# Performance work log

Measured on AMD Instinct MI355X. Metric: run time of the kernel, lower is better.

## Reference

```python
import jax, jax.numpy as jnp
import numpy as np

N = 8192
F_X = 48       # raw node feature dim
F_RW = 16      # random-walk feature dim
IN_DIM = F_X + F_RW   # 64
H1 = 128
H2 = 64
N_BRANCH = 4   # hop0 (identity) + hop1..hop3


def setup_inputs() -> dict:
    key = jax.random.key(0)
    ks = jax.random.split(key, 9)
    x = jax.random.normal(ks[0], (N, F_X), dtype=jnp.float32)
    walk_feats = jax.random.normal(ks[1], (N, F_RW), dtype=jnp.float32)
    hop1 = jax.random.uniform(ks[2], (N, N), dtype=jnp.float32)
    hop2 = jax.random.uniform(ks[3], (N, N), dtype=jnp.float32)
    hop3 = jax.random.uniform(ks[4], (N, N), dtype=jnp.float32)
    # Stacked params for the 4 parallel 2-layer MLPs (layer0..layer3)
    s1 = 1.0 / np.sqrt(IN_DIM)
    s2 = 1.0 / np.sqrt(H1)
    W1 = jax.random.uniform(ks[5], (N_BRANCH, IN_DIM, H1), dtype=jnp.float32, minval=-s1, maxval=s1)
    b1 = jax.random.uniform(ks[6], (N_BRANCH, H1), dtype=jnp.float32, minval=-s1, maxval=s1)
    W2 = jax.random.uniform(ks[7], (N_BRANCH, H1, H2), dtype=jnp.float32, minval=-s2, maxval=s2)
    b2 = jax.random.uniform(ks[8], (N_BRANCH, H2), dtype=jnp.float32, minval=-s2, maxval=s2)
    return {"x": x, "walk_feats": walk_feats, "hop1": hop1, "hop2": hop2,
            "hop3": hop3, "W1": W1, "b1": b1, "W2": W2, "b2": b2}


def reference(x, walk_feats, hop1, hop2, hop3, W1, b1, W2, b2):
    # X = cat(x, walk_feats) along feature dim (use_rw=True)
    X = jnp.concatenate([x, walk_feats], axis=1)          # [N, IN_DIM]
    # Branch inputs: hop0 uses X directly; hops 1-3 aggregate via adjacency matmul
    hops = jnp.stack([X, hop1 @ X, hop2 @ X, hop3 @ X])   # [4, N, IN_DIM]
    # Parallel 2-layer MLPs: Linear -> ReLU -> Linear, per branch k
    h = jax.nn.relu(jnp.einsum('knf,kfh->knh', hops, W1) + b1[:, None, :])  # [4, N, H1]
    out = jnp.einsum('knh,kho->kno', h, W2) + b2[:, None, :]                 # [4, N, H2]
    return out.sum(axis=0)                                                   # [N, H2]
```

## Files before the change

kernel.cpp:

```cpp
#include <hip/hip_runtime.h>
#include <stdint.h>


#define N_NODES 8192
#define NDIM 64

typedef __attribute__((ext_vector_type(8))) short short8;
typedef __attribute__((ext_vector_type(4))) float f32x4;

__device__ __forceinline__ unsigned int f2bf(float f) {
  unsigned int u = __builtin_bit_cast(unsigned int, f);
  u += 0x7fffu + ((u >> 16) & 1u);
  return u >> 16;
}

__global__ void prep_kernel(const float* __restrict__ x,
                            const float* __restrict__ wf,
                            unsigned short* __restrict__ Bp) {
  int s = blockIdx.x * 256 + threadIdx.x;
  int khi = s >> 9;
  int rem = s & 511;
  int n   = rem >> 3;
  int klo = rem & 7;
  int k   = (khi << 3) | klo;
  float v = (n < 48) ? x[k * 48 + n] : wf[k * 16 + (n - 48)];
  Bp[s] = (unsigned short)f2bf(v);
}

__global__ void hop_gemm(const float* __restrict__ hop1,
                         const float* __restrict__ hop2,
                         const float* __restrict__ hop3,
                         const unsigned short* __restrict__ Bp,
                         float* __restrict__ Y) {
  int bid  = blockIdx.x;
  int h    = bid % 3;
  int mblk = bid / 3;
  const float* A = (h == 0) ? hop1 : (h == 1) ? hop2 : hop3;

  int tid  = threadIdx.x;
  int wave = tid >> 6;
  int lane = tid & 63;
  int n0   = lane & 15;
  int q    = lane >> 4;

  int rowA = mblk * 32 + wave * 16 + n0;
  const float* Arow = A + (size_t)rowA * N_NODES + q * 8;
  const short8* Bp8 = (const short8*)Bp;

  f32x4 acc0 = {0.f, 0.f, 0.f, 0.f};
  f32x4 acc1 = {0.f, 0.f, 0.f, 0.f};
  f32x4 acc2 = {0.f, 0.f, 0.f, 0.f};
  f32x4 acc3 = {0.f, 0.f, 0.f, 0.f};

#pragma unroll 4
  for (int k0 = 0; k0 < N_NODES; k0 += 32) {
    float4 a0 = *(const float4*)(Arow + k0);
    float4 a1 = *(const float4*)(Arow + k0 + 4);
    union { short8 s; unsigned int u[4]; } af;
    af.u[0] = (f2bf(a0.y) << 16) | f2bf(a0.x);
    af.u[1] = (f2bf(a0.w) << 16) | f2bf(a0.z);
    af.u[2] = (f2bf(a1.y) << 16) | f2bf(a1.x);
    af.u[3] = (f2bf(a1.w) << 16) | f2bf(a1.z);

    int bc = ((k0 >> 3) + q) * 64 + n0;
    short8 b0 = Bp8[bc];
    short8 b1 = Bp8[bc + 16];
    short8 b2 = Bp8[bc + 32];
    short8 b3 = Bp8[bc + 48];

    acc0 = __builtin_amdgcn_mfma_f32_16x16x32_bf16(af.s, b0, acc0, 0, 0, 0);
    acc1 = __builtin_amdgcn_mfma_f32_16x16x32_bf16(af.s, b1, acc1, 0, 0, 0);
    acc2 = __builtin_amdgcn_mfma_f32_16x16x32_bf16(af.s, b2, acc2, 0, 0, 0);
    acc3 = __builtin_amdgcn_mfma_f32_16x16x32_bf16(af.s, b3, acc3, 0, 0, 0);
  }

  float* Yo = Y + (size_t)h * (N_NODES * NDIM);
  int rowT = mblk * 32 + wave * 16 + 4 * q;
#pragma unroll
  for (int r = 0; r < 4; ++r) {
    float* yr = Yo + (size_t)(rowT + r) * NDIM + n0;
    yr[0]  = acc0[r];
    yr[16] = acc1[r];
    yr[32] = acc2[r];
    yr[48] = acc3[r];
  }
}

__global__ __launch_bounds__(256) void mlp_kernel(
    const float* __restrict__ x, const float* __restrict__ wf,
    const float* __restrict__ Y,
    const float* __restrict__ W1, const float* __restrict__ b1,
    const float* __restrict__ W2, const float* __restrict__ b2,
    float* __restrict__ out) {
  __shared__ __attribute__((aligned(16))) float Ys[32 * 64];
  __shared__ __attribute__((aligned(16))) float Ws[128 * 64];
  __shared__ __attribute__((aligned(16))) float Hs[32 * 128];
  __shared__ __attribute__((aligned(16))) float b1s[128];
  __shared__ __attribute__((aligned(16))) float b2s[64];

  int t = threadIdx.x;
  int rowBase = blockIdx.x * 32;

  int rg = t >> 5;
  int fg = t & 31;
  int rg2 = t >> 4;
  int cg  = t & 15;

  float oacc[2][4];
#pragma unroll
  for (int i = 0; i < 2; ++i)
#pragma unroll
    for (int j = 0; j < 4; ++j) oacc[i][j] = 0.f;

  for (int k = 0; k < 4; ++k) {
    for (int i = t; i < 32 * 64; i += 256) {
      float v;
      if (k == 0) {
        int row = rowBase + (i >> 6);
        int n = i & 63;
        v = (n < 48) ? x[row * 48 + n] : wf[row * 16 + (n - 48)];
      } else {
        v = Y[(size_t)(k - 1) * (N_NODES * 64) + (size_t)rowBase * 64 + i];
      }
      Ys[i] = v;
    }
    for (int i = t; i < 8192; i += 256) Ws[i] = W1[k * 8192 + i];
    if (t < 128) b1s[t] = b1[k * 128 + t];
    if (t >= 128 && t < 192) b2s[t - 128] = b2[k * 64 + (t - 128)];
    __syncthreads();

    float4 hacc[4];
#pragma unroll
    for (int i = 0; i < 4; ++i) hacc[i] = make_float4(0.f, 0.f, 0.f, 0.f);
    for (int kk = 0; kk < 64; ++kk) {
      float4 wv = *(const float4*)&Ws[kk * 128 + fg * 4];
#pragma unroll
      for (int i = 0; i < 4; ++i) {
        float yv = Ys[(rg * 4 + i) * 64 + kk];
        hacc[i].x = fmaf(yv, wv.x, hacc[i].x);
        hacc[i].y = fmaf(yv, wv.y, hacc[i].y);
        hacc[i].z = fmaf(yv, wv.z, hacc[i].z);
        hacc[i].w = fmaf(yv, wv.w, hacc[i].w);
      }
    }
    float4 bv = *(const float4*)&b1s[fg * 4];
#pragma unroll
    for (int i = 0; i < 4; ++i) {
      float4 hv;
      hv.x = fmaxf(hacc[i].x + bv.x, 0.f);
      hv.y = fmaxf(hacc[i].y + bv.y, 0.f);
      hv.z = fmaxf(hacc[i].z + bv.z, 0.f);
      hv.w = fmaxf(hacc[i].w + bv.w, 0.f);
      *(float4*)&Hs[(rg * 4 + i) * 128 + fg * 4] = hv;
    }
    __syncthreads();

    for (int i = t; i < 8192; i += 256) Ws[i] = W2[k * 8192 + i];
    __syncthreads();

    float o[2][4];
#pragma unroll
    for (int i = 0; i < 2; ++i) {
      float4 b2v = *(const float4*)&b2s[cg * 4];
      o[i][0] = b2v.x; o[i][1] = b2v.y; o[i][2] = b2v.z; o[i][3] = b2v.w;
    }
    for (int kk = 0; kk < 128; ++kk) {
      float4 wv = *(const float4*)&Ws[kk * 64 + cg * 4];
#pragma unroll
      for (int i = 0; i < 2; ++i) {
        float hv = Hs[(rg2 * 2 + i) * 128 + kk];
        o[i][0] = fmaf(hv, wv.x, o[i][0]);
        o[i][1] = fmaf(hv, wv.y, o[i][1]);
        o[i][2] = fmaf(hv, wv.z, o[i][2]);
        o[i][3] = fmaf(hv, wv.w, o[i][3]);
      }
    }
#pragma unroll
    for (int i = 0; i < 2; ++i)
#pragma unroll
      for (int j = 0; j < 4; ++j) oacc[i][j] += o[i][j];
    __syncthreads();
  }

#pragma unroll
  for (int i = 0; i < 2; ++i) {
    float4 v;
    v.x = oacc[i][0]; v.y = oacc[i][1]; v.z = oacc[i][2]; v.w = oacc[i][3];
    *(float4*)&out[(size_t)(rowBase + rg2 * 2 + i) * 64 + cg * 4] = v;
  }
}

extern "C" void kernel_launch(void* const* d_in, const int* in_sizes, int n_in,
                              void* d_out, int out_size, void* d_ws, size_t ws_size,
                              hipStream_t stream) {
  const float* x    = (const float*)d_in[0];
  const float* wf   = (const float*)d_in[1];
  const float* hop1 = (const float*)d_in[2];
  const float* hop2 = (const float*)d_in[3];
  const float* hop3 = (const float*)d_in[4];
  const float* W1   = (const float*)d_in[5];
  const float* b1   = (const float*)d_in[6];
  const float* W2   = (const float*)d_in[7];
  const float* b2   = (const float*)d_in[8];
  float* out = (float*)d_out;

  unsigned short* Bp = (unsigned short*)d_ws;
  float* Y = (float*)((char*)d_ws + (1 << 20));

  prep_kernel<<<dim3(524288 / 256), dim3(256), 0, stream>>>(x, wf, Bp);
  hop_gemm<<<dim3(768), dim3(128), 0, stream>>>(hop1, hop2, hop3, Bp, Y);
  mlp_kernel<<<dim3(256), dim3(256), 0, stream>>>(x, wf, Y, W1, b1, W2, b2, out);
}
```

Measured before the change: 883.3 us.

## Split hop GEMM K across waves with LDS reduction and double-buffered loads

```diff
diff --git a/kernel.cpp b/kernel.cpp
--- a/kernel.cpp
+++ b/kernel.cpp
@@ -27,167 +27,195 @@
   Bp[s] = (unsigned short)f2bf(v);
 }
 
-__global__ void hop_gemm(const float* __restrict__ hop1,
-                         const float* __restrict__ hop2,
-                         const float* __restrict__ hop3,
-                         const unsigned short* __restrict__ Bp,
-                         float* __restrict__ Y) {
+__global__ __launch_bounds__(256, 6) void hop_gemm(
+    const float* __restrict__ hop1,
+    const float* __restrict__ hop2,
+    const float* __restrict__ hop3,
+    const unsigned short* __restrict__ Bp,
+    float* __restrict__ Y) {
+  __shared__ __attribute__((aligned(16))) float red[4 * 1024];
+
   int bid  = blockIdx.x;
   int h    = bid % 3;
   int mblk = bid / 3;
   const float* A = (h == 0) ? hop1 : (h == 1) ? hop2 : hop3;
 
   int tid  = threadIdx.x;
-  int wave = tid >> 6;
+  int w    = tid >> 6;
   int lane = tid & 63;
   int n0   = lane & 15;
   int q    = lane >> 4;
 
-  int rowA = mblk * 32 + wave * 16 + n0;
-  const float* Arow = A + (size_t)rowA * N_NODES + q * 8;
-  const short8* Bp8 = (const short8*)Bp;
+  int rowA = mblk * 16 + n0;
+  const float* Arow = A + (size_t)rowA * N_NODES + w * 2048 + q * 8;
+  const short8* Bw  = (const short8*)Bp + ((size_t)(w * 256 + q)) * 64 + n0;
 
   f32x4 acc0 = {0.f, 0.f, 0.f, 0.f};
   f32x4 acc1 = {0.f, 0.f, 0.f, 0.f};
   f32x4 acc2 = {0.f, 0.f, 0.f, 0.f};
   f32x4 acc3 = {0.f, 0.f, 0.f, 0.f};
 
-#pragma unroll 4
-  for (int k0 = 0; k0 < N_NODES; k0 += 32) {
-    float4 a0 = *(const float4*)(Arow + k0);
-    float4 a1 = *(const float4*)(Arow + k0 + 4);
-    union { short8 s; unsigned int u[4]; } af;
-    af.u[0] = (f2bf(a0.y) << 16) | f2bf(a0.x);
-    af.u[1] = (f2bf(a0.w) << 16) | f2bf(a0.z);
-    af.u[2] = (f2bf(a1.y) << 16) | f2bf(a1.x);
-    af.u[3] = (f2bf(a1.w) << 16) | f2bf(a1.z);
-
-    int bc = ((k0 >> 3) + q) * 64 + n0;
-    short8 b0 = Bp8[bc];
-    short8 b1 = Bp8[bc + 16];
-    short8 b2 = Bp8[bc + 32];
-    short8 b3 = Bp8[bc + 48];
-
-    acc0 = __builtin_amdgcn_mfma_f32_16x16x32_bf16(af.s, b0, acc0, 0, 0, 0);
-    acc1 = __builtin_amdgcn_mfma_f32_16x16x32_bf16(af.s, b1, acc1, 0, 0, 0);
-    acc2 = __builtin_amdgcn_mfma_f32_16x16x32_bf16(af.s, b2, acc2, 0, 0, 0);
-    acc3 = __builtin_amdgcn_mfma_f32_16x16x32_bf16(af.s, b3, acc3, 0, 0, 0);
-  }
-
-  float* Yo = Y + (size_t)h * (N_NODES * NDIM);
-  int rowT = mblk * 32 + wave * 16 + 4 * q;
-#pragma unroll
-  for (int r = 0; r < 4; ++r) {
-    float* yr = Yo + (size_t)(rowT + r) * NDIM + n0;
-    yr[0]  = acc0[r];
-    yr[16] = acc1[r];
-    yr[32] = acc2[r];
-    yr[48] = acc3[r];
-  }
-}
-
+  float4 xa0, xa1, ya0, ya1;
+  short8 xb0, xb1, xb2, xb3;
+  short8 yb0, yb1, yb2, yb3;
+
+#define LOAD_A(s, A0, A1)                                \
+  do {                                                   \
+    const float* _p = Arow + 32 * (s);                   \
+    A0 = *(const float4*)_p;                             \
+    A1 = *(const float4*)(_p + 4);                       \
+  } while (0)
+
+#define LOAD_B(s, B0, B1, B2, B3)                        \
+  do {                                                   \
+    const short8* _p = Bw + 256 * (s);                   \
+    B0 = _p[0]; B1 = _p[16]; B2 = _p[32]; B3 = _p[48];   \
+  } while (0)
+
+#define PROC(A0, A1, B0, B1, B2, B3)                                        \
+  do {                                                                      \
+    union { short8 s; unsigned int u[4]; } af;                              \
+    af.u[0] = (f2bf((A0).y) << 16) | f2bf((A0).x);                          \
+    af.u[1] = (f2bf((A0).w) << 16) | f2bf((A0).z);                          \
+    af.u[2] = (f2bf((A1).y) << 16) | f2bf((A1).x);                          \
+    af.u[3] = (f2bf((A1).w) << 16) | f2bf((A1).z);                          \
+    acc0 = __builtin_amdgcn_mfma_f32_16x16x32_bf16(af.s, B0, acc0, 0, 0, 0);\
+    acc1 = __builtin_amdgcn_mfma_f32_16x16x32_bf16(af.s, B1, acc1, 0, 0, 0);\
+    acc2 = __builtin_amdgcn_mfma_f32_16x16x32_bf16(af.s, B2, acc2, 0, 0, 0);\
+    acc3 = __builtin_amdgcn_mfma_f32_16x16x32_bf16(af.s, B3, acc3, 0, 0, 0);\
+  } while (0)
+
+  LOAD_A(0, xa0, xa1);
+  LOAD_B(0, xb0, xb1, xb2, xb3);
+#pragma unroll 1
+  for (int s = 0; s < 62; s += 2) {
+    LOAD_A(s + 1, ya0, ya1);
+    LOAD_B(s + 1, yb0, yb1, yb2, yb3);
+    PROC(xa0, xa1, xb0, xb1, xb2, xb3);
+    LOAD_A(s + 2, xa0, xa1);
+    LOAD_B(s + 2, xb0, xb1, xb2, xb3);
+    PROC(ya0, ya1, yb0, yb1, yb2, yb3);
+  }
+  LOAD_A(63, ya0, ya1);
+  LOAD_B(63, yb0, yb1, yb2, yb3);
+  PROC(xa0, xa1, xb0, xb1, xb2, xb3);
+  PROC(ya0, ya1, yb0, yb1, yb2, yb3);
+
+#undef LOAD_A
+#undef LOAD_B
+#undef PROC
+
+  {
+    float* rw = &red[w * 1024 + lane * 4];
+    *(f32x4*)(rw)       = acc0;
+    *(f32x4*)(rw + 256) = acc1;
+    *(f32x4*)(rw + 512) = acc2;
+    *(f32x4*)(rw + 768) = acc3;
+  }
+  __syncthreads();
+
+  {
+    int t = tid;
+    f32x4 v = *(const f32x4*)&red[t * 4];
+    v += *(const f32x4*)&red[1024 + t * 4];
+    v += *(const f32x4*)&red[2048 + t * 4];
+    v += *(const f32x4*)&red[3072 + t * 4];
+
+    int nt    = t >> 6;
+    int lane2 = t & 63;
+    int q2    = lane2 >> 4;
+    int n02   = lane2 & 15;
+    int col   = nt * 16 + n02;
+    float* Yo = Y + (size_t)h * (N_NODES * NDIM)
+                  + (size_t)(mblk * 16 + q2 * 4) * NDIM + col;
+    Yo[0 * NDIM] = v.x;
+    Yo[1 * NDIM] = v.y;
+    Yo[2 * NDIM] = v.z;
+    Yo[3 * NDIM] = v.w;
+  }
+}
+
+#define YS_LD 68
+#define HS_LD 132
 __global__ __launch_bounds__(256) void mlp_kernel(
     const float* __restrict__ x, const float* __restrict__ wf,
     const float* __restrict__ Y,
     const float* __restrict__ W1, const float* __restrict__ b1,
     const float* __restrict__ W2, const float* __restrict__ b2,
     float* __restrict__ out) {
-  __shared__ __attribute__((aligned(16))) float Ys[32 * 64];
-  __shared__ __attribute__((aligned(16))) float Ws[128 * 64];
-  __shared__ __attribute__((aligned(16))) float Hs[32 * 128];
-  __shared__ __attribute__((aligned(16))) float b1s[128];
-  __shared__ __attribute__((aligned(16))) float b2s[64];
+  __shared__ __attribute__((aligned(16))) float Ys[16 * YS_LD];
+  __shared__ __attribute__((aligned(16))) float Hs[16 * HS_LD];
+  __shared__ float b1s[128];
+  __shared__ float b2s[64];
 
   int t = threadIdx.x;
-  int rowBase = blockIdx.x * 32;
-
-  int rg = t >> 5;
-  int fg = t & 31;
-  int rg2 = t >> 4;
-  int cg  = t & 15;
-
-  float oacc[2][4];
-#pragma unroll
-  for (int i = 0; i < 2; ++i)
-#pragma unroll
-    for (int j = 0; j < 4; ++j) oacc[i][j] = 0.f;
+  int rowBase = blockIdx.x * 16;
+
+  int r  = t >> 4;
+  int c8 = (t & 15) * 8;
+  int c4 = (t & 15) * 4;
+
+  float oacc[4] = {0.f, 0.f, 0.f, 0.f};
 
   for (int k = 0; k < 4; ++k) {
-    for (int i = t; i < 32 * 64; i += 256) {
+    for (int i = t; i < 16 * 64; i += 256) {
+      int row = i >> 6;
+      int n   = i & 63;
       float v;
       if (k == 0) {
-        int row = rowBase + (i >> 6);
-        int n = i & 63;
-        v = (n < 48) ? x[row * 48 + n] : wf[row * 16 + (n - 48)];
+        int grow = rowBase + row;
+        v = (n < 48) ? x[grow * 48 + n] : wf[grow * 16 + (n - 48)];
       } else {
-        v = Y[(size_t)(k - 1) * (N_NODES * 64) + (size_t)rowBase * 64 + i];
+        v = Y[(size_t)(k - 1) * (N_NODES * 64) + (size_t)(rowBase + row) * 64 + n];
       }
-      Ys[i] = v;
-    }
-    for (int i = t; i < 8192; i += 256) Ws[i] = W1[k * 8192 + i];
+      Ys[row * YS_LD + n] = v;
+    }
     if (t < 128) b1s[t] = b1[k * 128 + t];
-    if (t >= 128 && t < 192) b2s[t - 128] = b2[k * 64 + (t - 128)];
+    else if (t < 192) b2s[t - 128] = b2[k * 64 + (t - 128)];
     __syncthreads();
 
-    float4 hacc[4];
-#pragma unroll
-    for (int i = 0; i < 4; ++i) hacc[i] = make_float4(0.f, 0.f, 0.f, 0.f);
+    const float* W1k = W1 + k * 8192;
+    float f0 = 0.f, f1 = 0.f, f2 = 0.f, f3 = 0.f;
+    float f4 = 0.f, f5 = 0.f, f6 = 0.f, f7 = 0.f;
+#pragma unroll 4
     for (int kk = 0; kk < 64; ++kk) {
-      float4 wv = *(const float4*)&Ws[kk * 128 + fg * 4];
-#pragma unroll
-      for (int i = 0; i < 4; ++i) {
-        float yv = Ys[(rg * 4 + i) * 64 + kk];
-        hacc[i].x = fmaf(yv, wv.x, hacc[i].x);
-        hacc[i].y = fmaf(yv, wv.y, hacc[i].y);
-        hacc[i].z = fmaf(yv, wv.z, hacc[i].z);
-        hacc[i].w = fmaf(yv, wv.w, hacc[i].w);
-      }
-    }
-    float4 bv = *(const float4*)&b1s[fg * 4];
-#pragma unroll
-    for (int i = 0; i < 4; ++i) {
-      float4 hv;
-      hv.x = fmaxf(hacc[i].x + bv.x, 0.f);
-      hv.y = fmaxf(hacc[i].y + bv.y, 0.f);
-      hv.z = fmaxf(hacc[i].z + bv.z, 0.f);
-      hv.w = fmaxf(hacc[i].w + bv.w, 0.f);
-      *(float4*)&Hs[(rg * 4 + i) * 128 + fg * 4] = hv;
+      float yv = Ys[r * YS_LD + kk];
+      float4 w0 = *(const float4*)&W1k[kk * 128 + c8];
+      float4 w1 = *(const float4*)&W1k[kk * 128 + c8 + 4];
+      f0 = fmaf(yv, w0.x, f0); f1 = fmaf(yv, w0.y, f1);
+      f2 = fmaf(yv, w0.z, f2); f3 = fmaf(yv, w0.w, f3);
+      f4 = fmaf(yv, w1.x, f4); f5 = fmaf(yv, w1.y, f5);
+      f6 = fmaf(yv, w1.z, f6); f7 = fmaf(yv, w1.w, f7);
+    }
+    {
+      float4 ba = *(const float4*)&b1s[c8];
+      float4 bb = *(const float4*)&b1s[c8 + 4];
+      float4 h0, h1;
+      h0.x = fmaxf(f0 + ba.x, 0.f); h0.y = fmaxf(f1 + ba.y, 0.f);
+      h0.z = fmaxf(f2 + ba.z, 0.f); h0.w = fmaxf(f3 + ba.w, 0.f);
+      h1.x = fmaxf(f4 + bb.x, 0.f); h1.y = fmaxf(f5 + bb.y, 0.f);
+      h1.z = fmaxf(f6 + bb.z, 0.f); h1.w = fmaxf(f7 + bb.w, 0.f);
+      *(float4*)&Hs[r * HS_LD + c8]     = h0;
+      *(float4*)&Hs[r * HS_LD + c8 + 4] = h1;
     }
     __syncthreads();
 
-    for (int i = t; i < 8192; i += 256) Ws[i] = W2[k * 8192 + i];
+    const float* W2k = W2 + k * 8192;
+    float o0 = b2s[c4], o1 = b2s[c4 + 1], o2 = b2s[c4 + 2], o3 = b2s[c4 + 3];
+#pragma unroll 4
+    for (int kk = 0; kk < 128; ++kk) {
+      float hv = Hs[r * HS_LD + kk];
+      float4 wv = *(const float4*)&W2k[kk * 64 + c4];
+      o0 = fmaf(hv, wv.x, o0); o1 = fmaf(hv, wv.y, o1);
+      o2 = fmaf(hv, wv.z, o2); o3 = fmaf(hv, wv.w, o3);
+    }
+    oacc[0] += o0; oacc[1] += o1; oacc[2] += o2; oacc[3] += o3;
     __syncthreads();
-
-    float o[2][4];
-#pragma unroll
-    for (int i = 0; i < 2; ++i) {
-      float4 b2v = *(const float4*)&b2s[cg * 4];
-      o[i][0] = b2v.x; o[i][1] = b2v.y; o[i][2] = b2v.z; o[i][3] = b2v.w;
-    }
-    for (int kk = 0; kk < 128; ++kk) {
-      float4 wv = *(const float4*)&Ws[kk * 64 + cg * 4];
-#pragma unroll
-      for (int i = 0; i < 2; ++i) {
-        float hv = Hs[(rg2 * 2 + i) * 128 + kk];
-        o[i][0] = fmaf(hv, wv.x, o[i][0]);
-        o[i][1] = fmaf(hv, wv.y, o[i][1]);
-        o[i][2] = fmaf(hv, wv.z, o[i][2]);
-        o[i][3] = fmaf(hv, wv.w, o[i][3]);
-      }
-    }
-#pragma unroll
-    for (int i = 0; i < 2; ++i)
-#pragma unroll
-      for (int j = 0; j < 4; ++j) oacc[i][j] += o[i][j];
-    __syncthreads();
-  }
-
-#pragma unroll
-  for (int i = 0; i < 2; ++i) {
-    float4 v;
-    v.x = oacc[i][0]; v.y = oacc[i][1]; v.z = oacc[i][2]; v.w = oacc[i][3];
-    *(float4*)&out[(size_t)(rowBase + rg2 * 2 + i) * 64 + cg * 4] = v;
-  }
+  }
+
+  float4 v;
+  v.x = oacc[0]; v.y = oacc[1]; v.z = oacc[2]; v.w = oacc[3];
+  *(float4*)&out[(size_t)(rowBase + r) * 64 + c4] = v;
 }
 
 extern "C" void kernel_launch(void* const* d_in, const int* in_sizes, int n_in,
@@ -208,6 +236,6 @@
   float* Y = (float*)((char*)d_ws + (1 << 20));
 
   prep_kernel<<<dim3(524288 / 256), dim3(256), 0, stream>>>(x, wf, Bp);
-  hop_gemm<<<dim3(768), dim3(128), 0, stream>>>(hop1, hop2, hop3, Bp, Y);
-  mlp_kernel<<<dim3(256), dim3(256), 0, stream>>>(x, wf, Y, W1, b1, W2, b2, out);
-}
+  hop_gemm<<<dim3(1536), dim3(256), 0, stream>>>(hop1, hop2, hop3, Bp, Y);
+  mlp_kernel<<<dim3(512), dim3(256), 0, stream>>>(x, wf, Y, W1, b1, W2, b2, out);
+}
```

New measurement: 808.2 us. 1.09x faster.
